# Performance work log

Hardware: AMD Instinct MI355X
Metric: run time of the kernel (lower is better)

Reference implementation:

```python
import jax, jax.numpy as jnp
import numpy as np

NODE_SIZE = 40000
REL_SIZE = 2000
TRIPLE_SIZE = 600000
DIM = 128
DEPTH = 2
EPS = 1e-12


def _xavier(key, shape):
    lim = np.sqrt(6.0 / (shape[-2] + shape[-1]))
    return jax.random.uniform(key, shape, minval=-lim, maxval=lim, dtype=jnp.float32)


def _l2norm(x):
    # matches torch F.normalize(p=2, eps=1e-12)
    return x / jnp.maximum(jnp.linalg.norm(x, axis=-1, keepdims=True), EPS)


def _sparse_softmax(row, vals, n_rows):
    # torch.sparse.softmax over nonzeros of each row
    m = jax.ops.segment_max(vals, row, num_segments=n_rows)
    e = jnp.exp(vals - m[row])
    s = jax.ops.segment_sum(e, row, num_segments=n_rows)
    return e / s[row]


def _avg(adj, emb, n_rows):
    # sparse_coo(ones) -> sparse softmax over rows -> sparse mm  (== mean over neighbors)
    row, col = adj[0], adj[1]
    w = _sparse_softmax(row, jnp.zeros(row.shape, emb.dtype), n_rows)  # softmax of equal values
    return jax.ops.segment_sum(w[:, None] * emb[col], row, num_segments=n_rows)


def _nr_encoder(features, rel_emb, adj, r_index, r_val, triple_size, rel_size, node_size,
                attn, gate, proxy, bias):
    # NR_GraphAttention (Dual-AMN style relational reflection attention)
    row, col = adj[0], adj[1]
    # per-triple relation embedding: sparse [T, R] @ rel_emb
    tri_rel = jax.ops.segment_sum(r_val[:, None] * rel_emb[r_index[1]], r_index[0],
                                  num_segments=triple_size)
    tri_rel = _l2norm(tri_rel)  # [T, DIM]
    feats = jnp.tanh(features)
    outs = [feats]
    for l in range(DEPTH):
        neighs = feats[col]                                            # gather [T, DIM]
        neighs = neighs - 2.0 * jnp.sum(neighs * tri_rel, axis=-1, keepdims=True) * tri_rel
        att = _sparse_softmax(row, tri_rel @ attn[l][:, 0], node_size)  # edge attention
        feats = jnp.tanh(jax.ops.segment_sum(neighs * att[:, None], row,
                                             num_segments=node_size))  # scatter-sum
        outs.append(feats)
    out = jnp.concatenate(outs, axis=-1)                               # [N, DIM*(DEPTH+1)]
    # proxy matching + gating
    pa = jax.nn.softmax(_l2norm(out) @ _l2norm(proxy).T, axis=-1)
    pf = out - pa @ proxy
    g = jax.nn.sigmoid(pf @ gate + bias)
    return g * out + (1.0 - g) * pf


def setup_inputs() -> dict:
    ks = jax.random.split(jax.random.key(0), 16)
    ent_adj = jax.random.randint(ks[0], (2, TRIPLE_SIZE), 0, NODE_SIZE, dtype=jnp.int32)
    rel_adj = jnp.stack([jax.random.randint(ks[1], (TRIPLE_SIZE,), 0, NODE_SIZE, dtype=jnp.int32),
                         jax.random.randint(ks[2], (TRIPLE_SIZE,), 0, REL_SIZE, dtype=jnp.int32)])
    adj_list = jax.random.randint(ks[3], (2, TRIPLE_SIZE), 0, NODE_SIZE, dtype=jnp.int32)
    r_index = jnp.stack([jnp.arange(TRIPLE_SIZE, dtype=jnp.int32),
                         jax.random.randint(ks[4], (TRIPLE_SIZE,), 0, REL_SIZE, dtype=jnp.int32)])
    r_val = jax.random.uniform(ks[5], (TRIPLE_SIZE,), dtype=jnp.float32)
    mask = jnp.ones((NODE_SIZE,), dtype=jnp.int32)
    F3 = DIM * (DEPTH + 1)
    return dict(
        ent_adj=ent_adj, rel_adj=rel_adj, node_size=NODE_SIZE, rel_size=REL_SIZE,
        adj_list=adj_list, r_index=r_index, r_val=r_val, triple_size=TRIPLE_SIZE, mask=mask,
        ent_emb=_xavier(ks[6], (NODE_SIZE, DIM)),
        rel_emb=_xavier(ks[7], (REL_SIZE, DIM)),
        e_attn=_xavier(ks[8], (DEPTH, DIM, 1)), e_gate=_xavier(ks[9], (F3, F3)),
        e_proxy=_xavier(ks[10], (64, F3)), e_bias=jnp.zeros((1, F3), jnp.float32),
        r_attn=_xavier(ks[11], (DEPTH, DIM, 1)), r_gate=_xavier(ks[12], (F3, F3)),
        r_proxy=_xavier(ks[13], (64, F3)), r_bias=jnp.zeros((1, F3), jnp.float32),
    )


def reference(ent_adj, rel_adj, node_size, rel_size, adj_list, r_index, r_val, triple_size, mask,
              ent_emb, rel_emb, e_attn, e_gate, e_proxy, e_bias,
              r_attn, r_gate, r_proxy, r_bias):
    ent_feature = _avg(ent_adj, ent_emb, node_size)   # [N, DIM]
    rel_feature = _avg(rel_adj, rel_emb, node_size)   # [N, DIM]
    ent_feat = _nr_encoder(ent_feature, rel_emb, adj_list, r_index, r_val,
                           triple_size, rel_size, node_size, e_attn, e_gate, e_proxy, e_bias)
    rel_feat = _nr_encoder(rel_feature, rel_emb, adj_list, r_index, r_val,
                           triple_size, rel_size, node_size, r_attn, r_gate, r_proxy, r_bias)
    # dropout_rate = 0.0 -> identity
    return jnp.concatenate([ent_feat, rel_feat], axis=-1)  # [N, 768]
```

## Files before the change

kernel.cpp:

```cpp
#include <hip/hip_runtime.h>
#include <cmath>

#define NNODE 40000
#define NREL  2000
#define NTRI  600000
#define DIMK  128
#define F3    384
#define NPROX 64
#define EPSN  1e-12f
#define NSLICE 8
#define SLICE_ROWS (NNODE / NSLICE)
#define NRP 313

typedef unsigned short ushort_t;
typedef __attribute__((ext_vector_type(8))) short bf16x8;
typedef __attribute__((ext_vector_type(4))) float f32x4;

static __device__ __forceinline__ float waveSum(float v) {
#pragma unroll
    for (int m = 32; m >= 1; m >>= 1) v += __shfl_xor(v, m, 64);
    return v;
}

static __device__ __forceinline__ void qreduce4(float4& v) {
#pragma unroll
    for (int m = 16; m <= 32; m <<= 1) {
        v.x += __shfl_xor(v.x, m, 64);
        v.y += __shfl_xor(v.y, m, 64);
        v.z += __shfl_xor(v.z, m, 64);
        v.w += __shfl_xor(v.w, m, 64);
    }
}

static __device__ __forceinline__ uint2 splitpair(float x, float y) {
    unsigned int bx = __float_as_uint(x), by = __float_as_uint(y);
    unsigned int h = (bx >> 16) | (by & 0xffff0000u);
    float lx = x - __uint_as_float(bx & 0xffff0000u);
    float ly = y - __uint_as_float(by & 0xffff0000u);
    unsigned int l = (__float_as_uint(lx) >> 16) | (__float_as_uint(ly) & 0xffff0000u);
    return make_uint2(h, l);
}

static __device__ __forceinline__ void pack8(const float4& a, const float4& b,
                                             uint4& h, uint4& l) {
    uint2 p0 = splitpair(a.x, a.y);
    uint2 p1 = splitpair(a.z, a.w);
    uint2 p2 = splitpair(b.x, b.y);
    uint2 p3 = splitpair(b.z, b.w);
    h = make_uint4(p0.x, p1.x, p2.x, p3.x);
    l = make_uint4(p0.y, p1.y, p2.y, p3.y);
}

__global__ void k_count3(const int* __restrict__ rA, const int* __restrict__ rE,
                         const int* __restrict__ rR, int* __restrict__ dA,
                         int* __restrict__ dE, int* __restrict__ dR) {
    int t = blockIdx.x * 256 + threadIdx.x;
    if (t < NTRI) {
        atomicAdd(&dA[rA[t]], 1);
        atomicAdd(&dE[rE[t]], 1);
        atomicAdd(&dR[rR[t]], 1);
    }
}

__global__ void k_scan_fast(const int* __restrict__ dA, int* __restrict__ oA,
                            const int* __restrict__ dE, int* __restrict__ oE,
                            const int* __restrict__ dR, int* __restrict__ oR) {
    const int* deg = blockIdx.x == 0 ? dA : (blockIdx.x == 1 ? dE : dR);
    int* off = blockIdx.x == 0 ? oA : (blockIdx.x == 1 ? oE : oR);
    __shared__ int wsum[16];
    __shared__ int wpre[16];
    int tid = threadIdx.x;
    int lane = tid & 63, wv = tid >> 6;
    const int CH = 40;
    int base = tid * CH;
    int s = 0;
    for (int i = 0; i < CH; i++) {
        int idx = base + i;
        s += (idx < NNODE) ? deg[idx] : 0;
    }
    int incl = s;
#pragma unroll
    for (int m = 1; m < 64; m <<= 1) {
        int v = __shfl_up(incl, m, 64);
        if (lane >= m) incl += v;
    }
    if (lane == 63) wsum[wv] = incl;
    __syncthreads();
    if (tid < 16) {
        int v = wsum[tid];
#pragma unroll
        for (int m = 1; m < 16; m <<= 1) {
            int u = __shfl_up(v, m, 64);
            if (tid >= m) v += u;
        }
        wpre[tid] = v;
    }
    __syncthreads();
    int waveoff = (wv == 0) ? 0 : wpre[wv - 1];
    int run = waveoff + incl - s;
    for (int i = 0; i < CH; i++) {
        int idx = base + i;
        if (idx < NNODE) {
            off[idx] = run;
            run += deg[idx];
        }
    }
    if (tid == 0) off[NNODE] = wpre[15];
}

__global__ __launch_bounds__(256) void k_place_sliced(
    const int* __restrict__ rA, const int* __restrict__ cA,
    const int* __restrict__ rE, const int* __restrict__ cE,
    const int* __restrict__ rR, const int* __restrict__ cR,
    const int* __restrict__ ridx, const float* __restrict__ rval,
    const float* __restrict__ nrm,
    const int* __restrict__ oA, const int* __restrict__ oE, const int* __restrict__ oR,
    int* __restrict__ cntA, int* __restrict__ cntE, int* __restrict__ cntR,
    int2* __restrict__ ePackSc, int* __restrict__ eColE, int* __restrict__ eColR) {
    int slice = blockIdx.x & (NSLICE - 1);
    int t = (blockIdx.x >> 3) * 256 + threadIdx.x;
    if (t >= NTRI) return;
    int lo = slice * SLICE_ROWS;
    int r = rA[t];
    if ((unsigned)(r - lo) < (unsigned)SLICE_ROWS) {
        int rid = ridx[t];
        float v = rval[t];
        float sc = v / fmaxf(fabsf(v) * nrm[rid], EPSN);
        int p = oA[r] + atomicAdd(&cntA[r], 1);
        ePackSc[p] = make_int2(cA[t] | (rid << 16), __float_as_int(sc));
    }
    r = rE[t];
    if ((unsigned)(r - lo) < (unsigned)SLICE_ROWS)
        eColE[oE[r] + atomicAdd(&cntE[r], 1)] = cE[t];
    r = rR[t];
    if ((unsigned)(r - lo) < (unsigned)SLICE_ROWS)
        eColR[oR[r] + atomicAdd(&cntR[r], 1)] = cR[t];
}

__global__ void k_relprep(const float* __restrict__ rel_emb,
                          const float* __restrict__ e_attn, const float* __restrict__ r_attn,
                          float* __restrict__ nrm, float2* __restrict__ attL0,
                          float2* __restrict__ attL1) {
    int r = blockIdx.x;
    int lane = threadIdx.x;
    float a = rel_emb[r * DIMK + lane];
    float b = rel_emb[r * DIMK + 64 + lane];
    float nn = waveSum(a * a + b * b);
    float d0 = waveSum(a * e_attn[lane] + b * e_attn[64 + lane]);
    float d1 = waveSum(a * e_attn[DIMK + lane] + b * e_attn[DIMK + 64 + lane]);
    float d2 = waveSum(a * r_attn[lane] + b * r_attn[64 + lane]);
    float d3 = waveSum(a * r_attn[DIMK + lane] + b * r_attn[DIMK + 64 + lane]);
    if (lane == 0) {
        nrm[r] = sqrtf(nn);
        attL0[r] = make_float2(d0, d2);
        attL1[r] = make_float2(d1, d3);
    }
}

__global__ void k_proxyprep2(const float* __restrict__ e_proxy, const float* __restrict__ r_proxy,
                             float* __restrict__ pnT_e, float* __restrict__ pnT_r) {
    int enc = blockIdx.x >= NPROX;
    int k = blockIdx.x & (NPROX - 1);
    const float* proxy = enc ? r_proxy : e_proxy;
    float* pnT = enc ? pnT_r : pnT_e;
    int lane = threadIdx.x;
    float v[6];
    float ss = 0.f;
#pragma unroll
    for (int j = 0; j < 6; j++) {
        v[j] = proxy[k * F3 + j * 64 + lane];
        ss += v[j] * v[j];
    }
    ss = waveSum(ss);
    float inv = 1.0f / fmaxf(sqrtf(ss), EPSN);
#pragma unroll
    for (int j = 0; j < 6; j++) pnT[(j * 64 + lane) * NPROX + k] = v[j] * inv;
}

__global__ void k_gateprep2(const float* __restrict__ e_gate, const float* __restrict__ r_gate,
                            ushort_t* __restrict__ the, ushort_t* __restrict__ tle,
                            ushort_t* __restrict__ thr, ushort_t* __restrict__ tlr) {
    int enc = blockIdx.x >= F3;
    int k = enc ? blockIdx.x - F3 : blockIdx.x;
    const float* g = enc ? r_gate : e_gate;
    ushort_t* th = enc ? thr : the;
    ushort_t* tl = enc ? tlr : tle;
    int c = threadIdx.x;
    float v = g[(size_t)k * F3 + c];
    unsigned int b = __float_as_uint(v);
    th[(size_t)c * F3 + k] = (ushort_t)(b >> 16);
    float lo = v - __uint_as_float(b & 0xffff0000u);
    tl[(size_t)c * F3 + k] = (ushort_t)(__float_as_uint(lo) >> 16);
}

__global__ void k_pgprep(const float* __restrict__ e_proxy, const float* __restrict__ r_proxy,
                         const float* __restrict__ e_gate, const float* __restrict__ r_gate,
                         ushort_t* __restrict__ pgTh_e, ushort_t* __restrict__ pgTl_e,
                         ushort_t* __restrict__ prTh_e, ushort_t* __restrict__ prTl_e,
                         ushort_t* __restrict__ pgTh_r, ushort_t* __restrict__ pgTl_r,
                         ushort_t* __restrict__ prTh_r, ushort_t* __restrict__ prTl_r) {
    int enc = blockIdx.y;
    const float* proxy = enc ? r_proxy : e_proxy;
    const float* gate = enc ? r_gate : e_gate;
    ushort_t* pgTh = enc ? pgTh_r : pgTh_e;
    ushort_t* pgTl = enc ? pgTl_r : pgTl_e;
    ushort_t* prTh = enc ? prTh_r : prTh_e;
    ushort_t* prTl = enc ? prTl_r : prTl_e;
    int c = blockIdx.x;
    int p = threadIdx.x;
    float s = 0.f;
    for (int k = 0; k < F3; k++) s = fmaf(proxy[p * F3 + k], gate[(size_t)k * F3 + c], s);
    float v = -s;
    unsigned int b = __float_as_uint(v);
    pgTh[c * NPROX + p] = (ushort_t)(b >> 16);
    float lo = v - __uint_as_float(b & 0xffff0000u);
    pgTl[c * NPROX + p] = (ushort_t)(__float_as_uint(lo) >> 16);
    float pv = proxy[p * F3 + c];
    unsigned int pb = __float_as_uint(pv);
    prTh[c * NPROX + p] = (ushort_t)(pb >> 16);
    float plo = pv - __uint_as_float(pb & 0xffff0000u);
    prTl[c * NPROX + p] = (ushort_t)(__float_as_uint(plo) >> 16);
}

__global__ __launch_bounds__(256) void k_avg2(
    const int* __restrict__ offE, const int* __restrict__ eColE, const float* __restrict__ ent_emb,
    const int* __restrict__ offR, const int* __restrict__ eColR, const float* __restrict__ rel_emb,
    float* __restrict__ out_e, float* __restrict__ out_r) {
    int gw = (blockIdx.x * blockDim.x + threadIdx.x) >> 6;
    int lane = threadIdx.x & 63;
    if (gw >= 2 * NNODE) return;
    bool isR = gw >= NNODE;
    int wid = isR ? gw - NNODE : gw;
    const int* off = isR ? offR : offE;
    const int* ecol = isR ? eColR : eColE;
    const float4* emb4 = (const float4*)(isR ? rel_emb : ent_emb);
    float* outp = isR ? out_r : out_e;
    int q = lane >> 4, ql = lane & 15;
    int e0 = off[wid], e1 = off[wid + 1];
    float4 aA = {0, 0, 0, 0}, aB = {0, 0, 0, 0};
    for (int base = e0; base < e1; base += 64) {
        int n = min(64, e1 - base);
        int mc = (lane < n) ? ecol[base + lane] : -1;
        for (int j = 0; j < n; j += 4) {
            int e = j + q;
            int c = __shfl(mc, e, 64);
            if (e < n) {
                float4 va = emb4[(size_t)c * 32 + ql];
                float4 vb = emb4[(size_t)c * 32 + 16 + ql];
                aA.x += va.x; aA.y += va.y; aA.z += va.z; aA.w += va.w;
                aB.x += vb.x; aB.y += vb.y; aB.z += vb.z; aB.w += vb.w;
            }
        }
    }
    qreduce4(aA);
    qreduce4(aB);
    if (q == 0) {
        float invd = (e1 > e0) ? 1.0f / (float)(e1 - e0) : 0.0f;
        float4* o = (float4*)outp;
        float4 ra = {tanhf(aA.x * invd), tanhf(aA.y * invd), tanhf(aA.z * invd), tanhf(aA.w * invd)};
        float4 rb = {tanhf(aB.x * invd), tanhf(aB.y * invd), tanhf(aB.z * invd), tanhf(aB.w * invd)};
        o[(size_t)wid * 96 + ql] = ra;
        o[(size_t)wid * 96 + 16 + ql] = rb;
    }
}

__global__ __launch_bounds__(256) void k_agg2(
    const int* __restrict__ off, const int2* __restrict__ ePackSc,
    const float2* __restrict__ attL, const float* __restrict__ rel_emb,
    float* __restrict__ out_e, float* __restrict__ out_r, int lin) {
    int wid = (blockIdx.x * blockDim.x + threadIdx.x) >> 6;
    int lane = threadIdx.x & 63;
    if (wid >= NNODE) return;
    int q = lane >> 4, ql = lane & 15;
    int e0 = off[wid], e1 = off[wid + 1];
    const float4* rel4 = (const float4*)rel_emb;
    const float4* pe4 = (const float4*)out_e;
    const float4* pr4 = (const float4*)out_r;
    int sA = lin * 32 + ql, sB = lin * 32 + 16 + ql;
    float4 aEa = {0, 0, 0, 0}, aEb = {0, 0, 0, 0}, aRa = {0, 0, 0, 0}, aRb = {0, 0, 0, 0};
    float sE = 0.f, sR = 0.f;
    for (int base = e0; base < e1; base += 64) {
        int n = min(64, e1 - base);
        int pk = 0;
        float sc = 0.f, wE = 0.f, wR = 0.f;
        if (lane < n) {
            int2 ps = ePackSc[base + lane];
            pk = ps.x;
            sc = __int_as_float(ps.y);
            float2 a = attL[pk >> 16];
            wE = __expf(sc * a.x);
            wR = __expf(sc * a.y);
        }
        for (int j = 0; j < n; j += 4) {
            int e = j + q;
            int pke = __shfl(pk, e, 64);
            float sce = __shfl(sc, e, 64);
            float wEe = __shfl(wE, e, 64);
            float wRe = __shfl(wR, e, 64);
            int c = pke & 0xFFFF;
            int r = pke >> 16;
            float4 ra = rel4[(size_t)r * 32 + ql];
            float4 rb = rel4[(size_t)r * 32 + 16 + ql];
            float4 fa = pe4[(size_t)c * 96 + sA];
            float4 fb = pe4[(size_t)c * 96 + sB];
            float4 ga = pr4[(size_t)c * 96 + sA];
            float4 gb = pr4[(size_t)c * 96 + sB];
            float tax = sce * ra.x, tay = sce * ra.y, taz = sce * ra.z, taw = sce * ra.w;
            float tbx = sce * rb.x, tby = sce * rb.y, tbz = sce * rb.z, tbw = sce * rb.w;
            float dE = fa.x * tax + fa.y * tay + fa.z * taz + fa.w * taw +
                       fb.x * tbx + fb.y * tby + fb.z * tbz + fb.w * tbw;
            float dR = ga.x * tax + ga.y * tay + ga.z * taz + ga.w * taw +
                       gb.x * tbx + gb.y * tby + gb.z * tbz + gb.w * tbw;
#pragma unroll
            for (int m = 1; m <= 8; m <<= 1) {
                dE += __shfl_xor(dE, m, 64);
                dR += __shfl_xor(dR, m, 64);
            }
            dE *= 2.f;
            dR *= 2.f;
            aEa.x += wEe * (fa.x - dE * tax);
            aEa.y += wEe * (fa.y - dE * tay);
            aEa.z += wEe * (fa.z - dE * taz);
            aEa.w += wEe * (fa.w - dE * taw);
            aEb.x += wEe * (fb.x - dE * tbx);
            aEb.y += wEe * (fb.y - dE * tby);
            aEb.z += wEe * (fb.z - dE * tbz);
            aEb.w += wEe * (fb.w - dE * tbw);
            aRa.x += wRe * (ga.x - dR * tax);
            aRa.y += wRe * (ga.y - dR * tay);
            aRa.z += wRe * (ga.z - dR * taz);
            aRa.w += wRe * (ga.w - dR * taw);
            aRb.x += wRe * (gb.x - dR * tbx);
            aRb.y += wRe * (gb.y - dR * tby);
            aRb.z += wRe * (gb.z - dR * tbz);
            aRb.w += wRe * (gb.w - dR * tbw);
            sE += wEe;
            sR += wRe;
        }
    }
    qreduce4(aEa);
    qreduce4(aEb);
    qreduce4(aRa);
    qreduce4(aRb);
#pragma unroll
    for (int m = 16; m <= 32; m <<= 1) {
        sE += __shfl_xor(sE, m, 64);
        sR += __shfl_xor(sR, m, 64);
    }
    if (q == 0) {
        float iE = (e1 > e0) ? 1.f / sE : 0.f;
        float4* o = (float4*)out_e;
        float4 wa = {tanhf(aEa.x * iE), tanhf(aEa.y * iE), tanhf(aEa.z * iE), tanhf(aEa.w * iE)};
        float4 wb = {tanhf(aEb.x * iE), tanhf(aEb.y * iE), tanhf(aEb.z * iE), tanhf(aEb.w * iE)};
        o[(size_t)wid * 96 + (lin + 1) * 32 + ql] = wa;
        o[(size_t)wid * 96 + (lin + 1) * 32 + 16 + ql] = wb;
    } else if (q == 1) {
        float iR = (e1 > e0) ? 1.f / sR : 0.f;
        float4* o = (float4*)out_r;
        float4 wa = {tanhf(aRa.x * iR), tanhf(aRa.y * iR), tanhf(aRa.z * iR), tanhf(aRa.w * iR)};
        float4 wb = {tanhf(aRb.x * iR), tanhf(aRb.y * iR), tanhf(aRb.z * iR), tanhf(aRb.w * iR)};
        o[(size_t)wid * 96 + (lin + 1) * 32 + ql] = wa;
        o[(size_t)wid * 96 + (lin + 1) * 32 + 16 + ql] = wb;
    }
}

__global__ void k_scores(const float* __restrict__ out_e, const float* __restrict__ out_r,
                         const float* __restrict__ pnT_e, const float* __restrict__ pnT_r,
                         ushort_t* __restrict__ paH_e, ushort_t* __restrict__ paL_e,
                         ushort_t* __restrict__ paH_r, ushort_t* __restrict__ paL_r) {
    const float* outb = blockIdx.z ? out_r : out_e;
    const float* pnT = blockIdx.z ? pnT_r : pnT_e;
    ushort_t* paH = blockIdx.z ? paH_r : paH_e;
    ushort_t* paL = blockIdx.z ? paL_r : paL_e;
    __shared__ __align__(16) float As[16][68];
    __shared__ __align__(16) float Bs[16][68];
    __shared__ float Ss[64][65];
    __shared__ float rnS[64];
    int tid = threadIdx.x;
    int row0 = blockIdx.x * 64;
    int kk = tid & 15, rr = tid >> 4;
    int cb = tid & 63, kb = tid >> 6;
    int tx = tid & 15, ty = tid >> 4;
    int c0 = tx * 4, r0 = ty * 4;
    float acc[4][4] = {};
    float ssp[4] = {};
    for (int k0 = 0; k0 < F3; k0 += 16) {
#pragma unroll
        for (int u = 0; u < 4; u++) {
            int r = rr + u * 16;
            float v = outb[(size_t)(row0 + r) * F3 + k0 + kk];
            As[kk][r] = v;
            ssp[u] += v * v;
        }
#pragma unroll
        for (int u = 0; u < 4; u++) {
            int k = kb + u * 4;
            Bs[k][cb] = pnT[(size_t)(k0 + k) * NPROX + cb];
        }
        __syncthreads();
#pragma unroll
        for (int k = 0; k < 16; k++) {
            float4 av = *(const float4*)&As[k][r0];
            float4 bv = *(const float4*)&Bs[k][c0];
            float a[4] = {av.x, av.y, av.z, av.w};
            float b[4] = {bv.x, bv.y, bv.z, bv.w};
#pragma unroll
            for (int i = 0; i < 4; i++)
#pragma unroll
                for (int j = 0; j < 4; j++) acc[i][j] += a[i] * b[j];
        }
        __syncthreads();
    }
#pragma unroll
    for (int u = 0; u < 4; u++) {
        float ss = ssp[u];
#pragma unroll
        for (int m = 1; m < 16; m <<= 1) ss += __shfl_xor(ss, m, 64);
        if (kk == 0) rnS[rr + u * 16] = 1.0f / fmaxf(sqrtf(ss), EPSN);
    }
    __syncthreads();
#pragma unroll
    for (int i = 0; i < 4; i++) {
        float rn = rnS[r0 + i];
#pragma unroll
        for (int j = 0; j < 4; j++) Ss[r0 + i][c0 + j] = acc[i][j] * rn;
    }
    __syncthreads();
    if (tid < 64) {
        int r = tid;
        float m = -1e30f;
        for (int c = 0; c < 64; c++) m = fmaxf(m, Ss[r][c]);
        float s = 0.f;
        for (int c = 0; c < 64; c++) s += expf(Ss[r][c] - m);
        float inv = 1.f / s;
        size_t base = (size_t)(row0 + r) * NPROX;
        for (int c = 0; c < 64; c++) {
            float v = expf(Ss[r][c] - m) * inv;
            unsigned int b = __float_as_uint(v);
            paH[base + c] = (ushort_t)(b >> 16);
            float lo = v - __uint_as_float(b & 0xffff0000u);
            paL[base + c] = (ushort_t)(__float_as_uint(lo) >> 16);
        }
    }
}

__global__ __launch_bounds__(256) void k_gate_fused(
    const ushort_t* __restrict__ paH_e, const ushort_t* __restrict__ paL_e,
    const ushort_t* __restrict__ paH_r, const ushort_t* __restrict__ paL_r,
    const ushort_t* __restrict__ gTh_e, const ushort_t* __restrict__ gTl_e,
    const ushort_t* __restrict__ gTh_r, const ushort_t* __restrict__ gTl_r,
    const ushort_t* __restrict__ pgTh_e, const ushort_t* __restrict__ pgTl_e,
    const ushort_t* __restrict__ prTh_e, const ushort_t* __restrict__ prTl_e,
    const ushort_t* __restrict__ pgTh_r, const ushort_t* __restrict__ pgTl_r,
    const ushort_t* __restrict__ prTh_r, const ushort_t* __restrict__ prTl_r,
    const float* __restrict__ e_bias, const float* __restrict__ r_bias,
    const float* __restrict__ out_e, const float* __restrict__ out_r,
    float* __restrict__ dout) {
    int id = blockIdx.x;
    int slot = id >> 3;
    int rp = (id & 7) + (slot / 12) * 8;
    int v = slot % 12;
    int ctile = v >> 1;
    int z = v & 1;
    if (rp >= NRP) return;
    const ushort_t* paH = z ? paH_r : paH_e;
    const ushort_t* paL = z ? paL_r : paL_e;
    const ushort_t* gTh = z ? gTh_r : gTh_e;
    const ushort_t* gTl = z ? gTl_r : gTl_e;
    const ushort_t* pgTh = z ? pgTh_r : pgTh_e;
    const ushort_t* pgTl = z ? pgTl_r : pgTl_e;
    const ushort_t* prTh = z ? prTh_r : prTh_e;
    const ushort_t* prTl = z ? prTl_r : prTl_e;
    const float* bias = z ? r_bias : e_bias;
    const float* outb = z ? out_r : out_e;
    int outoff = z ? F3 : 0;
    __shared__ __align__(16) ushort_t AsH[128 * 40];
    __shared__ __align__(16) ushort_t AsL[128 * 40];
    int tid = threadIdx.x;
    int w = tid >> 6, lane = tid & 63;
    int quad = lane >> 4, l16 = lane & 15;
    int wrow = (w >> 1) * 64, wcol = (w & 1) * 32;
    int gr0 = rp * 128;
    int cb0 = ctile * 64;
    f32x4 accg[4][2], accp[4][2];
#pragma unroll
    for (int rt = 0; rt < 4; rt++)
#pragma unroll
        for (int ct = 0; ct < 2; ct++) {
            accg[rt][ct] = (f32x4){0.f, 0.f, 0.f, 0.f};
            accp[rt][ct] = (f32x4){0.f, 0.f, 0.f, 0.f};
        }

    int srow = tid >> 2, sseg = tid & 3;
    int gr_u0 = gr0 + srow;
    int gr_u1 = gr0 + srow + 64;
    float4 p0a, p0b, p1a, p1b;
    {
        float4 zv = {0, 0, 0, 0};
        p0a = p0b = p1a = p1b = zv;
        if (gr_u0 < NNODE) {
            p0a = *(const float4*)&outb[(size_t)gr_u0 * F3 + sseg * 8];
            p0b = *(const float4*)&outb[(size_t)gr_u0 * F3 + sseg * 8 + 4];
        }
        if (gr_u1 < NNODE) {
            p1a = *(const float4*)&outb[(size_t)gr_u1 * F3 + sseg * 8];
            p1b = *(const float4*)&outb[(size_t)gr_u1 * F3 + sseg * 8 + 4];
        }
    }
    for (int k0 = 0; k0 < F3; k0 += 32) {
        __syncthreads();
        uint4 h0, l0, h1, l1;
        pack8(p0a, p0b, h0, l0);
        pack8(p1a, p1b, h1, l1);
        *(uint4*)&AsH[srow * 40 + sseg * 8] = h0;
        *(uint4*)&AsL[srow * 40 + sseg * 8] = l0;
        *(uint4*)&AsH[(srow + 64) * 40 + sseg * 8] = h1;
        *(uint4*)&AsL[(srow + 64) * 40 + sseg * 8] = l1;
        bf16x8 bh[2], bl[2];
#pragma unroll
        for (int ct = 0; ct < 2; ct++) {
            int bc = cb0 + wcol + ct * 16 + l16;
            bh[ct] = *(const bf16x8*)&gTh[(size_t)bc * F3 + k0 + quad * 8];
            bl[ct] = *(const bf16x8*)&gTl[(size_t)bc * F3 + k0 + quad * 8];
        }
        int kn = k0 + 32;
        if (kn < F3) {
            if (gr_u0 < NNODE) {
                p0a = *(const float4*)&outb[(size_t)gr_u0 * F3 + kn + sseg * 8];
                p0b = *(const float4*)&outb[(size_t)gr_u0 * F3 + kn + sseg * 8 + 4];
            }
            if (gr_u1 < NNODE) {
                p1a = *(const float4*)&outb[(size_t)gr_u1 * F3 + kn + sseg * 8];
                p1b = *(const float4*)&outb[(size_t)gr_u1 * F3 + kn + sseg * 8 + 4];
            }
        }
        __syncthreads();
        bf16x8 ah[4], al[4];
#pragma unroll
        for (int rt = 0; rt < 4; rt++) {
            int ar = wrow + rt * 16 + l16;
            ah[rt] = *(const bf16x8*)&AsH[ar * 40 + quad * 8];
            al[rt] = *(const bf16x8*)&AsL[ar * 40 + quad * 8];
        }
#pragma unroll
        for (int rt = 0; rt < 4; rt++)
#pragma unroll
            for (int ct = 0; ct < 2; ct++) {
                accg[rt][ct] = __builtin_amdgcn_mfma_f32_16x16x32_bf16(ah[rt], bh[ct], accg[rt][ct], 0, 0, 0);
                accg[rt][ct] = __builtin_amdgcn_mfma_f32_16x16x32_bf16(ah[rt], bl[ct], accg[rt][ct], 0, 0, 0);
                accg[rt][ct] = __builtin_amdgcn_mfma_f32_16x16x32_bf16(al[rt], bh[ct], accg[rt][ct], 0, 0, 0);
            }
    }
    const bf16x8 zz = (bf16x8){0, 0, 0, 0, 0, 0, 0, 0};
#pragma unroll
    for (int kp = 0; kp < 2; kp++) {
        int kp0 = kp * 32;
        bf16x8 pah[4], pal[4];
#pragma unroll
        for (int rt = 0; rt < 4; rt++) {
            int ar = gr0 + wrow + rt * 16 + l16;
            if (ar < NNODE) {
                pah[rt] = *(const bf16x8*)&paH[(size_t)ar * NPROX + kp0 + quad * 8];
                pal[rt] = *(const bf16x8*)&paL[(size_t)ar * NPROX + kp0 + quad * 8];
            } else {
                pah[rt] = zz;
                pal[rt] = zz;
            }
        }
        bf16x8 pgh[2], pgl[2], prh[2], prl[2];
#pragma unroll
        for (int ct = 0; ct < 2; ct++) {
            int bc = cb0 + wcol + ct * 16 + l16;
            pgh[ct] = *(const bf16x8*)&pgTh[(size_t)bc * NPROX + kp0 + quad * 8];
            pgl[ct] = *(const bf16x8*)&pgTl[(size_t)bc * NPROX + kp0 + quad * 8];
            prh[ct] = *(const bf16x8*)&prTh[(size_t)bc * NPROX + kp0 + quad * 8];
            prl[ct] = *(const bf16x8*)&prTl[(size_t)bc * NPROX + kp0 + quad * 8];
        }
#pragma unroll
        for (int rt = 0; rt < 4; rt++)
#pragma unroll
            for (int ct = 0; ct < 2; ct++) {
                accg[rt][ct] = __builtin_amdgcn_mfma_f32_16x16x32_bf16(pah[rt], pgh[ct], accg[rt][ct], 0, 0, 0);
                accg[rt][ct] = __builtin_amdgcn_mfma_f32_16x16x32_bf16(pah[rt], pgl[ct], accg[rt][ct], 0, 0, 0);
                accg[rt][ct] = __builtin_amdgcn_mfma_f32_16x16x32_bf16(pal[rt], pgh[ct], accg[rt][ct], 0, 0, 0);
                accp[rt][ct] = __builtin_amdgcn_mfma_f32_16x16x32_bf16(pah[rt], prh[ct], accp[rt][ct], 0, 0, 0);
                accp[rt][ct] = __builtin_amdgcn_mfma_f32_16x16x32_bf16(pah[rt], prl[ct], accp[rt][ct], 0, 0, 0);
                accp[rt][ct] = __builtin_amdgcn_mfma_f32_16x16x32_bf16(pal[rt], prh[ct], accp[rt][ct], 0, 0, 0);
            }
    }
#pragma unroll
    for (int rt = 0; rt < 4; rt++) {
        int rbase = gr0 + wrow + rt * 16 + quad * 4;
#pragma unroll
        for (int reg = 0; reg < 4; reg++) {
            int row = rbase + reg;
            if (row >= NNODE) continue;
#pragma unroll
            for (int ct = 0; ct < 2; ct++) {
                int c = cb0 + wcol + ct * 16 + l16;
                float x = accg[rt][ct][reg] + bias[c];
                float g = 1.f / (1.f + __expf(-x));
                float o = outb[(size_t)row * F3 + c];
                float zp = accp[rt][ct][reg];
                dout[(size_t)row * 768 + outoff + c] = o - (1.f - g) * zp;
            }
        }
    }
}

extern "C" void kernel_launch(void* const* d_in, const int* in_sizes, int n_in,
                              void* d_out, int out_size, void* d_ws, size_t ws_size,
                              hipStream_t stream) {
    const int* ent_adj = (const int*)d_in[0];
    const int* rel_adj = (const int*)d_in[1];
    const int* adj_list = (const int*)d_in[4];
    const int* r_index = (const int*)d_in[5];
    const float* r_val = (const float*)d_in[6];
    const float* ent_emb = (const float*)d_in[9];
    const float* rel_emb = (const float*)d_in[10];
    const float* e_attn = (const float*)d_in[11];
    const float* e_gate = (const float*)d_in[12];
    const float* e_proxy = (const float*)d_in[13];
    const float* e_bias = (const float*)d_in[14];
    const float* r_attn = (const float*)d_in[15];
    const float* r_gate = (const float*)d_in[16];
    const float* r_proxy = (const float*)d_in[17];
    const float* r_bias = (const float*)d_in[18];
    float* out = (float*)d_out;

    char* ws = (char*)d_ws;
    size_t off = 0;
    auto alloc = [&](size_t bytes) -> void* {
        off = (off + 255) & ~(size_t)255;
        void* p = ws + off;
        off += bytes;
        return p;
    };

    int* degcur = (int*)alloc(6 * NNODE * sizeof(int));
    int* degA = degcur, *curA = degcur + NNODE;
    int* degE = degcur + 2 * NNODE, *curE = degcur + 3 * NNODE;
    int* degR = degcur + 4 * NNODE, *curR = degcur + 5 * NNODE;
    int* offA = (int*)alloc((NNODE + 1) * sizeof(int));
    int* offE = (int*)alloc((NNODE + 1) * sizeof(int));
    int* offR = (int*)alloc((NNODE + 1) * sizeof(int));
    int2* ePackSc = (int2*)alloc(NTRI * sizeof(int2));
    int* eColE = (int*)alloc(NTRI * sizeof(int));
    int* eColR = (int*)alloc(NTRI * sizeof(int));
    float* nrm = (float*)alloc(NREL * sizeof(float));
    float2* attL0 = (float2*)alloc(NREL * sizeof(float2));
    float2* attL1 = (float2*)alloc(NREL * sizeof(float2));
    float* pnT_e = (float*)alloc((size_t)F3 * NPROX * sizeof(float));
    float* pnT_r = (float*)alloc((size_t)F3 * NPROX * sizeof(float));
    ushort_t* gTh_e = (ushort_t*)alloc((size_t)F3 * F3 * sizeof(ushort_t));
    ushort_t* gTl_e = (ushort_t*)alloc((size_t)F3 * F3 * sizeof(ushort_t));
    ushort_t* gTh_r = (ushort_t*)alloc((size_t)F3 * F3 * sizeof(ushort_t));
    ushort_t* gTl_r = (ushort_t*)alloc((size_t)F3 * F3 * sizeof(ushort_t));
    ushort_t* pgTh_e = (ushort_t*)alloc((size_t)F3 * NPROX * sizeof(ushort_t));
    ushort_t* pgTl_e = (ushort_t*)alloc((size_t)F3 * NPROX * sizeof(ushort_t));
    ushort_t* prTh_e = (ushort_t*)alloc((size_t)F3 * NPROX * sizeof(ushort_t));
    ushort_t* prTl_e = (ushort_t*)alloc((size_t)F3 * NPROX * sizeof(ushort_t));
    ushort_t* pgTh_r = (ushort_t*)alloc((size_t)F3 * NPROX * sizeof(ushort_t));
    ushort_t* pgTl_r = (ushort_t*)alloc((size_t)F3 * NPROX * sizeof(ushort_t));
    ushort_t* prTh_r = (ushort_t*)alloc((size_t)F3 * NPROX * sizeof(ushort_t));
    ushort_t* prTl_r = (ushort_t*)alloc((size_t)F3 * NPROX * sizeof(ushort_t));
    ushort_t* paH_e = (ushort_t*)alloc((size_t)NNODE * NPROX * sizeof(ushort_t));
    ushort_t* paL_e = (ushort_t*)alloc((size_t)NNODE * NPROX * sizeof(ushort_t));
    ushort_t* paH_r = (ushort_t*)alloc((size_t)NNODE * NPROX * sizeof(ushort_t));
    ushort_t* paL_r = (ushort_t*)alloc((size_t)NNODE * NPROX * sizeof(ushort_t));
    float* out_e = (float*)alloc((size_t)NNODE * F3 * sizeof(float));
    float* out_r = (float*)alloc((size_t)NNODE * F3 * sizeof(float));
    (void)ws_size; (void)in_sizes; (void)n_in; (void)out_size;

    hipMemsetAsync(degcur, 0, 6 * NNODE * sizeof(int), stream);

    int gT = (NTRI + 255) / 256;
    k_count3<<<gT, 256, 0, stream>>>(adj_list, ent_adj, rel_adj, degA, degE, degR);
    k_scan_fast<<<3, 1024, 0, stream>>>(degA, offA, degE, offE, degR, offR);
    k_relprep<<<NREL, 64, 0, stream>>>(rel_emb, e_attn, r_attn, nrm, attL0, attL1);
    k_place_sliced<<<gT * NSLICE, 256, 0, stream>>>(
        adj_list, adj_list + NTRI, ent_adj, ent_adj + NTRI, rel_adj, rel_adj + NTRI,
        r_index + NTRI, r_val, nrm, offA, offE, offR, curA, curE, curR,
        ePackSc, eColE, eColR);
    k_proxyprep2<<<2 * NPROX, 64, 0, stream>>>(e_proxy, r_proxy, pnT_e, pnT_r);
    k_gateprep2<<<2 * F3, F3, 0, stream>>>(e_gate, r_gate, gTh_e, gTl_e, gTh_r, gTl_r);
    k_pgprep<<<dim3(F3, 2), 64, 0, stream>>>(e_proxy, r_proxy, e_gate, r_gate,
                                             pgTh_e, pgTl_e, prTh_e, prTl_e,
                                             pgTh_r, pgTl_r, prTh_r, prTl_r);

    k_avg2<<<(2 * NNODE) / 4, 256, 0, stream>>>(offE, eColE, ent_emb, offR, eColR, rel_emb,
                                                out_e, out_r);

    int gW = NNODE / 4;
    k_agg2<<<gW, 256, 0, stream>>>(offA, ePackSc, attL0, rel_emb, out_e, out_r, 0);
    k_agg2<<<gW, 256, 0, stream>>>(offA, ePackSc, attL1, rel_emb, out_e, out_r, 1);

    dim3 gS(NNODE / 64, 1, 2);
    k_scores<<<gS, 256, 0, stream>>>(out_e, out_r, pnT_e, pnT_r,
                                     paH_e, paL_e, paH_r, paL_r);
    k_gate_fused<<<3840, 256, 0, stream>>>(paH_e, paL_e, paH_r, paL_r,
                                           gTh_e, gTl_e, gTh_r, gTl_r,
                                           pgTh_e, pgTl_e, prTh_e, prTl_e,
                                           pgTh_r, pgTl_r, prTh_r, prTl_r,
                                           e_bias, r_bias, out_e, out_r, out);
}
```

Baseline: 935.2 us.

## Precompute bf16 hi/lo splits of features in producers; widen gate GEMM K-tile

The avg and aggregation kernels now also write bf16 high/low split copies of each output feature row. The fused gate kernel loads these pre-split values straight into shared memory instead of re-splitting fp32 features inside its K loop, and its K step grows from 32 to 64, which halves the number of barrier pairs. This removes repeated split arithmetic from the GEMM main loop. The cost is extra global writes and workspace (four N×384 ushort arrays) in the producers, and larger shared-memory tiles that may lower occupancy.

New measurement: 996.4 us. 6.5% more time.

```diff
diff --git a/kernel.cpp b/kernel.cpp
--- a/kernel.cpp
+++ b/kernel.cpp
@@ -41,14 +41,11 @@
     return make_uint2(h, l);
 }
 
-static __device__ __forceinline__ void pack8(const float4& a, const float4& b,
-                                             uint4& h, uint4& l) {
+static __device__ __forceinline__ void split4(const float4& a, uint2& h, uint2& l) {
     uint2 p0 = splitpair(a.x, a.y);
     uint2 p1 = splitpair(a.z, a.w);
-    uint2 p2 = splitpair(b.x, b.y);
-    uint2 p3 = splitpair(b.z, b.w);
-    h = make_uint4(p0.x, p1.x, p2.x, p3.x);
-    l = make_uint4(p0.y, p1.y, p2.y, p3.y);
+    h = make_uint2(p0.x, p1.x);
+    l = make_uint2(p0.y, p1.y);
 }
 
 __global__ void k_count3(const int* __restrict__ rA, const int* __restrict__ rE,
@@ -225,7 +222,9 @@
 __global__ __launch_bounds__(256) void k_avg2(
     const int* __restrict__ offE, const int* __restrict__ eColE, const float* __restrict__ ent_emb,
     const int* __restrict__ offR, const int* __restrict__ eColR, const float* __restrict__ rel_emb,
-    float* __restrict__ out_e, float* __restrict__ out_r) {
+    float* __restrict__ out_e, float* __restrict__ out_r,
+    ushort_t* __restrict__ outH_e, ushort_t* __restrict__ outL_e,
+    ushort_t* __restrict__ outH_r, ushort_t* __restrict__ outL_r) {
     int gw = (blockIdx.x * blockDim.x + threadIdx.x) >> 6;
     int lane = threadIdx.x & 63;
     if (gw >= 2 * NNODE) return;
@@ -235,6 +234,8 @@
     const int* ecol = isR ? eColR : eColE;
     const float4* emb4 = (const float4*)(isR ? rel_emb : ent_emb);
     float* outp = isR ? out_r : out_e;
+    ushort_t* outH = isR ? outH_r : outH_e;
+    ushort_t* outL = isR ? outL_r : outL_e;
     int q = lane >> 4, ql = lane & 15;
     int e0 = off[wid], e1 = off[wid + 1];
     float4 aA = {0, 0, 0, 0}, aB = {0, 0, 0, 0};
@@ -261,13 +262,22 @@
         float4 rb = {tanhf(aB.x * invd), tanhf(aB.y * invd), tanhf(aB.z * invd), tanhf(aB.w * invd)};
         o[(size_t)wid * 96 + ql] = ra;
         o[(size_t)wid * 96 + 16 + ql] = rb;
+        uint2 h, l;
+        split4(ra, h, l);
+        *(uint2*)&outH[(size_t)wid * F3 + ql * 4] = h;
+        *(uint2*)&outL[(size_t)wid * F3 + ql * 4] = l;
+        split4(rb, h, l);
+        *(uint2*)&outH[(size_t)wid * F3 + 64 + ql * 4] = h;
+        *(uint2*)&outL[(size_t)wid * F3 + 64 + ql * 4] = l;
     }
 }
 
 __global__ __launch_bounds__(256) void k_agg2(
     const int* __restrict__ off, const int2* __restrict__ ePackSc,
     const float2* __restrict__ attL, const float* __restrict__ rel_emb,
-    float* __restrict__ out_e, float* __restrict__ out_r, int lin) {
+    float* __restrict__ out_e, float* __restrict__ out_r,
+    ushort_t* __restrict__ outH_e, ushort_t* __restrict__ outL_e,
+    ushort_t* __restrict__ outH_r, ushort_t* __restrict__ outL_r, int lin) {
     int wid = (blockIdx.x * blockDim.x + threadIdx.x) >> 6;
     int lane = threadIdx.x & 63;
     if (wid >= NNODE) return;
@@ -347,6 +357,7 @@
         sE += __shfl_xor(sE, m, 64);
         sR += __shfl_xor(sR, m, 64);
     }
+    int col0 = (lin + 1) * 128 + ql * 4;
     if (q == 0) {
         float iE = (e1 > e0) ? 1.f / sE : 0.f;
         float4* o = (float4*)out_e;
@@ -354,6 +365,13 @@
         float4 wb = {tanhf(aEb.x * iE), tanhf(aEb.y * iE), tanhf(aEb.z * iE), tanhf(aEb.w * iE)};
         o[(size_t)wid * 96 + (lin + 1) * 32 + ql] = wa;
         o[(size_t)wid * 96 + (lin + 1) * 32 + 16 + ql] = wb;
+        uint2 h, l;
+        split4(wa, h, l);
+        *(uint2*)&outH_e[(size_t)wid * F3 + col0] = h;
+        *(uint2*)&outL_e[(size_t)wid * F3 + col0] = l;
+        split4(wb, h, l);
+        *(uint2*)&outH_e[(size_t)wid * F3 + col0 + 64] = h;
+        *(uint2*)&outL_e[(size_t)wid * F3 + col0 + 64] = l;
     } else if (q == 1) {
         float iR = (e1 > e0) ? 1.f / sR : 0.f;
         float4* o = (float4*)out_r;
@@ -361,6 +379,13 @@
         float4 wb = {tanhf(aRb.x * iR), tanhf(aRb.y * iR), tanhf(aRb.z * iR), tanhf(aRb.w * iR)};
         o[(size_t)wid * 96 + (lin + 1) * 32 + ql] = wa;
         o[(size_t)wid * 96 + (lin + 1) * 32 + 16 + ql] = wb;
+        uint2 h, l;
+        split4(wa, h, l);
+        *(uint2*)&outH_r[(size_t)wid * F3 + col0] = h;
+        *(uint2*)&outL_r[(size_t)wid * F3 + col0] = l;
+        split4(wb, h, l);
+        *(uint2*)&outH_r[(size_t)wid * F3 + col0 + 64] = h;
+        *(uint2*)&outL_r[(size_t)wid * F3 + col0 + 64] = l;
     }
 }
 
@@ -453,6 +478,8 @@
     const ushort_t* __restrict__ prTh_e, const ushort_t* __restrict__ prTl_e,
     const ushort_t* __restrict__ pgTh_r, const ushort_t* __restrict__ pgTl_r,
     const ushort_t* __restrict__ prTh_r, const ushort_t* __restrict__ prTl_r,
+    const ushort_t* __restrict__ outH_e, const ushort_t* __restrict__ outL_e,
+    const ushort_t* __restrict__ outH_r, const ushort_t* __restrict__ outL_r,
     const float* __restrict__ e_bias, const float* __restrict__ r_bias,
     const float* __restrict__ out_e, const float* __restrict__ out_r,
     float* __restrict__ dout) {
@@ -471,11 +498,13 @@
     const ushort_t* pgTl = z ? pgTl_r : pgTl_e;
     const ushort_t* prTh = z ? prTh_r : prTh_e;
     const ushort_t* prTl = z ? prTl_r : prTl_e;
+    const ushort_t* outH = z ? outH_r : outH_e;
+    const ushort_t* outL = z ? outL_r : outL_e;
     const float* bias = z ? r_bias : e_bias;
     const float* outb = z ? out_r : out_e;
     int outoff = z ? F3 : 0;
-    __shared__ __align__(16) ushort_t AsH[128 * 40];
-    __shared__ __align__(16) ushort_t AsL[128 * 40];
+    __shared__ __align__(16) ushort_t AsH[128 * 72];
+    __shared__ __align__(16) ushort_t AsL[128 * 72];
     int tid = threadIdx.x;
     int w = tid >> 6, lane = tid & 63;
     int quad = lane >> 4, l16 = lane & 15;
@@ -494,62 +523,73 @@
     int srow = tid >> 2, sseg = tid & 3;
     int gr_u0 = gr0 + srow;
     int gr_u1 = gr0 + srow + 64;
-    float4 p0a, p0b, p1a, p1b;
-    {
-        float4 zv = {0, 0, 0, 0};
-        p0a = p0b = p1a = p1b = zv;
-        if (gr_u0 < NNODE) {
-            p0a = *(const float4*)&outb[(size_t)gr_u0 * F3 + sseg * 8];
-            p0b = *(const float4*)&outb[(size_t)gr_u0 * F3 + sseg * 8 + 4];
-        }
-        if (gr_u1 < NNODE) {
-            p1a = *(const float4*)&outb[(size_t)gr_u1 * F3 + sseg * 8];
-            p1b = *(const float4*)&outb[(size_t)gr_u1 * F3 + sseg * 8 + 4];
-        }
-    }
-    for (int k0 = 0; k0 < F3; k0 += 32) {
+    bool v0 = gr_u0 < NNODE, v1 = gr_u1 < NNODE;
+    const ushort_t* h0p = &outH[(size_t)(v0 ? gr_u0 : 0) * F3 + sseg * 16];
+    const ushort_t* l0p = &outL[(size_t)(v0 ? gr_u0 : 0) * F3 + sseg * 16];
+    const ushort_t* h1p = &outH[(size_t)(v1 ? gr_u1 : 0) * F3 + sseg * 16];
+    const ushort_t* l1p = &outL[(size_t)(v1 ? gr_u1 : 0) * F3 + sseg * 16];
+    uint4 z4 = {0, 0, 0, 0};
+    uint4 rh0a, rh0b, rl0a, rl0b, rh1a, rh1b, rl1a, rl1b;
+    rh0a = v0 ? *(const uint4*)&h0p[0] : z4;
+    rh0b = v0 ? *(const uint4*)&h0p[8] : z4;
+    rl0a = v0 ? *(const uint4*)&l0p[0] : z4;
+    rl0b = v0 ? *(const uint4*)&l0p[8] : z4;
+    rh1a = v1 ? *(const uint4*)&h1p[0] : z4;
+    rh1b = v1 ? *(const uint4*)&h1p[8] : z4;
+    rl1a = v1 ? *(const uint4*)&l1p[0] : z4;
+    rl1b = v1 ? *(const uint4*)&l1p[8] : z4;
+    int sb0 = srow * 72 + sseg * 16;
+    int sb1 = (srow + 64) * 72 + sseg * 16;
+    for (int t = 0; t < 6; t++) {
+        int k0 = t * 64;
         __syncthreads();
-        uint4 h0, l0, h1, l1;
-        pack8(p0a, p0b, h0, l0);
-        pack8(p1a, p1b, h1, l1);
-        *(uint4*)&AsH[srow * 40 + sseg * 8] = h0;
-        *(uint4*)&AsL[srow * 40 + sseg * 8] = l0;
-        *(uint4*)&AsH[(srow + 64) * 40 + sseg * 8] = h1;
-        *(uint4*)&AsL[(srow + 64) * 40 + sseg * 8] = l1;
-        bf16x8 bh[2], bl[2];
-#pragma unroll
-        for (int ct = 0; ct < 2; ct++) {
-            int bc = cb0 + wcol + ct * 16 + l16;
-            bh[ct] = *(const bf16x8*)&gTh[(size_t)bc * F3 + k0 + quad * 8];
-            bl[ct] = *(const bf16x8*)&gTl[(size_t)bc * F3 + k0 + quad * 8];
-        }
-        int kn = k0 + 32;
+        *(uint4*)&AsH[sb0] = rh0a;
+        *(uint4*)&AsH[sb0 + 8] = rh0b;
+        *(uint4*)&AsL[sb0] = rl0a;
+        *(uint4*)&AsL[sb0 + 8] = rl0b;
+        *(uint4*)&AsH[sb1] = rh1a;
+        *(uint4*)&AsH[sb1 + 8] = rh1b;
+        *(uint4*)&AsL[sb1] = rl1a;
+        *(uint4*)&AsL[sb1 + 8] = rl1b;
+        bf16x8 bh[2][2], bl[2][2];
+#pragma unroll
+        for (int half = 0; half < 2; half++)
+#pragma unroll
+            for (int ct = 0; ct < 2; ct++) {
+                int bc = cb0 + wcol + ct * 16 + l16;
+                bh[half][ct] = *(const bf16x8*)&gTh[(size_t)bc * F3 + k0 + half * 32 + quad * 8];
+                bl[half][ct] = *(const bf16x8*)&gTl[(size_t)bc * F3 + k0 + half * 32 + quad * 8];
+            }
+        int kn = k0 + 64;
         if (kn < F3) {
-            if (gr_u0 < NNODE) {
-                p0a = *(const float4*)&outb[(size_t)gr_u0 * F3 + kn + sseg * 8];
-                p0b = *(const float4*)&outb[(size_t)gr_u0 * F3 + kn + sseg * 8 + 4];
+            rh0a = v0 ? *(const uint4*)&h0p[kn] : z4;
+            rh0b = v0 ? *(const uint4*)&h0p[kn + 8] : z4;
+            rl0a = v0 ? *(const uint4*)&l0p[kn] : z4;
+            rl0b = v0 ? *(const uint4*)&l0p[kn + 8] : z4;
+            rh1a = v1 ? *(const uint4*)&h1p[kn] : z4;
+            rh1b = v1 ? *(const uint4*)&h1p[kn + 8] : z4;
+            rl1a = v1 ? *(const uint4*)&l1p[kn] : z4;
+            rl1b = v1 ? *(const uint4*)&l1p[kn + 8] : z4;
+        }
+        __syncthreads();
+#pragma unroll
+        for (int half = 0; half < 2; half++) {
+            bf16x8 ah[4], al[4];
+#pragma unroll
+            for (int rt = 0; rt < 4; rt++) {
+                int ar = wrow + rt * 16 + l16;
+                ah[rt] = *(const bf16x8*)&AsH[ar * 72 + half * 32 + quad * 8];
+                al[rt] = *(const bf16x8*)&AsL[ar * 72 + half * 32 + quad * 8];
             }
-            if (gr_u1 < NNODE) {
-                p1a = *(const float4*)&outb[(size_t)gr_u1 * F3 + kn + sseg * 8];
-                p1b = *(const float4*)&outb[(size_t)gr_u1 * F3 + kn + sseg * 8 + 4];
-            }
-        }
-        __syncthreads();
-        bf16x8 ah[4], al[4];
-#pragma unroll
-        for (int rt = 0; rt < 4; rt++) {
-            int ar = wrow + rt * 16 + l16;
-            ah[rt] = *(const bf16x8*)&AsH[ar * 40 + quad * 8];
-            al[rt] = *(const bf16x8*)&AsL[ar * 40 + quad * 8];
-        }
-#pragma unroll
-        for (int rt = 0; rt < 4; rt++)
-#pragma unroll
-            for (int ct = 0; ct < 2; ct++) {
-                accg[rt][ct] = __builtin_amdgcn_mfma_f32_16x16x32_bf16(ah[rt], bh[ct], accg[rt][ct], 0, 0, 0);
-                accg[rt][ct] = __builtin_amdgcn_mfma_f32_16x16x32_bf16(ah[rt], bl[ct], accg[rt][ct], 0, 0, 0);
-                accg[rt][ct] = __builtin_amdgcn_mfma_f32_16x16x32_bf16(al[rt], bh[ct], accg[rt][ct], 0, 0, 0);
-            }
+#pragma unroll
+            for (int rt = 0; rt < 4; rt++)
+#pragma unroll
+                for (int ct = 0; ct < 2; ct++) {
+                    accg[rt][ct] = __builtin_amdgcn_mfma_f32_16x16x32_bf16(ah[rt], bh[half][ct], accg[rt][ct], 0, 0, 0);
+                    accg[rt][ct] = __builtin_amdgcn_mfma_f32_16x16x32_bf16(ah[rt], bl[half][ct], accg[rt][ct], 0, 0, 0);
+                    accg[rt][ct] = __builtin_amdgcn_mfma_f32_16x16x32_bf16(al[rt], bh[half][ct], accg[rt][ct], 0, 0, 0);
+                }
+        }
     }
     const bf16x8 zz = (bf16x8){0, 0, 0, 0, 0, 0, 0, 0};
 #pragma unroll
@@ -670,6 +710,10 @@
     ushort_t* paL_r = (ushort_t*)alloc((size_t)NNODE * NPROX * sizeof(ushort_t));
     float* out_e = (float*)alloc((size_t)NNODE * F3 * sizeof(float));
     float* out_r = (float*)alloc((size_t)NNODE * F3 * sizeof(float));
+    ushort_t* outH_e = (ushort_t*)alloc((size_t)NNODE * F3 * sizeof(ushort_t));
+    ushort_t* outL_e = (ushort_t*)alloc((size_t)NNODE * F3 * sizeof(ushort_t));
+    ushort_t* outH_r = (ushort_t*)alloc((size_t)NNODE * F3 * sizeof(ushort_t));
+    ushort_t* outL_r = (ushort_t*)alloc((size_t)NNODE * F3 * sizeof(ushort_t));
     (void)ws_size; (void)in_sizes; (void)n_in; (void)out_size;
 
     hipMemsetAsync(degcur, 0, 6 * NNODE * sizeof(int), stream);
@@ -689,11 +733,14 @@
                                              pgTh_r, pgTl_r, prTh_r, prTl_r);
 
     k_avg2<<<(2 * NNODE) / 4, 256, 0, stream>>>(offE, eColE, ent_emb, offR, eColR, rel_emb,
-                                                out_e, out_r);
+                                                out_e, out_r,
+                                                outH_e, outL_e, outH_r, outL_r);
 
     int gW = NNODE / 4;
-    k_agg2<<<gW, 256, 0, stream>>>(offA, ePackSc, attL0, rel_emb, out_e, out_r, 0);
-    k_agg2<<<gW, 256, 0, stream>>>(offA, ePackSc, attL1, rel_emb, out_e, out_r, 1);
+    k_agg2<<<gW, 256, 0, stream>>>(offA, ePackSc, attL0, rel_emb, out_e, out_r,
+                                   outH_e, outL_e, outH_r, outL_r, 0);
+    k_agg2<<<gW, 256, 0, stream>>>(offA, ePackSc, attL1, rel_emb, out_e, out_r,
+                                   outH_e, outL_e, outH_r, outL_r, 1);
 
     dim3 gS(NNODE / 64, 1, 2);
     k_scores<<<gS, 256, 0, stream>>>(out_e, out_r, pnT_e, pnT_r,
@@ -702,5 +749,6 @@
                                            gTh_e, gTl_e, gTh_r, gTl_r,
                                            pgTh_e, pgTl_e, prTh_e, prTl_e,
                                            pgTh_r, pgTl_r, prTh_r, prTl_r,
+                                           outH_e, outL_e, outH_r, outL_r,
                                            e_bias, r_bias, out_e, out_r, out);
 }
```
